# Performance work log

Measured on AMD Instinct MI355X. Metric: run time of the kernel, lower is better.

## Reference

```python
import jax, jax.numpy as jnp
import numpy as np

B, N, C, H, P = 16, 4096, 256, 4, 64  # batch, tokens, hidden, heads, proj_size
HD = C // H  # head dim = 64
EPS = 1e-12  # torch F.normalize eps


def _l2norm(t):
    # normalize along last axis, torch-style: t / max(||t||, eps)
    n = jnp.sqrt(jnp.sum(t * t, axis=-1, keepdims=True))
    return t / jnp.maximum(n, EPS)


def setup_inputs() -> dict:
    key = jax.random.key(0)
    ks = jax.random.split(key, 12)
    s = 0.02
    return {
        "x": jax.random.normal(ks[0], (B, N, C), jnp.float32),
        "ref": jax.random.normal(ks[1], (B, N, C), jnp.float32),
        "Wq": jax.random.normal(ks[2], (C, C), jnp.float32) * s,
        "bq": jnp.zeros((C,), jnp.float32),
        "Wkvv": jax.random.normal(ks[3], (3 * C, C), jnp.float32) * s,
        "bkvv": jnp.zeros((3 * C,), jnp.float32),
        "WE": jax.random.normal(ks[4], (P, N), jnp.float32) * s,  # E and F share weights
        "bE": jnp.zeros((P,), jnp.float32),
        "Wo1": jax.random.normal(ks[5], (C // 2, C), jnp.float32) * s,
        "bo1": jnp.zeros((C // 2,), jnp.float32),
        "Wo2": jax.random.normal(ks[6], (C // 2, C), jnp.float32) * s,
        "bo2": jnp.zeros((C // 2,), jnp.float32),
        "temp": jnp.ones((H, 1, 1), jnp.float32),
        "temp2": jnp.ones((H, 1, 1), jnp.float32),
    }


def reference(x, ref, Wq, bq, Wkvv, bkvv, WE, bE, Wo1, bo1, Wo2, bo2, temp, temp2):
    b, n, c = x.shape
    hd = c // H
    # q projection -> [B,H,hd,N] (already transposed so channel dim first)
    q = (x @ Wq.T + bq).reshape(b, n, H, hd).transpose(0, 2, 3, 1)
    kvv = (ref @ Wkvv.T + bkvv).reshape(b, n, 3, H, hd).transpose(2, 0, 3, 4, 1)
    k, v_ca, v_sa = kvv[0], kvv[1], kvv[2]
    # L2 normalize over token axis (last)
    qn = _l2norm(q)
    kn = _l2norm(k)
    # ---- channel attention (XCA-style): [B,H,hd,hd]
    attn_ca = jax.nn.softmax(jnp.einsum('bhcn,bhdn->bhcd', qn, kn) * temp, axis=-1)
    x_ca = jnp.einsum('bhcd,bhdn->bhcn', attn_ca, v_ca)  # [B,H,hd,N]
    x_ca = x_ca.transpose(0, 3, 1, 2).reshape(b, n, c)   # [B,N,C]
    # ---- spatial attention with Linformer-style projection (E == F shared)
    k_proj = kn @ WE.T + bE      # [B,H,hd,P]
    v_proj = v_sa @ WE.T + bE    # [B,H,hd,P]
    attn_sa = jax.nn.softmax(jnp.einsum('bhcn,bhcp->bhnp', qn, k_proj) * temp2, axis=-1)
    x_sa = jnp.einsum('bhnp,bhcp->bhnc', attn_sa, v_proj)  # [B,H,N,hd]
    # faithful to original permute(0,3,1,2).reshape(B,N,C)
    x_sa = x_sa.transpose(0, 3, 1, 2).reshape(b, n, c)
    # output projections + concat (SA first, then CA)
    out_ca = x_ca @ Wo1.T + bo1
    out_sa = x_sa @ Wo2.T + bo2
    return jnp.concatenate((out_sa, out_ca), axis=-1)
```

## Files before the change

kernel.cpp:

```cpp
#include <hip/hip_runtime.h>
#include <hip/hip_bf16.h>

#define DI __device__ __forceinline__

constexpr int B_ = 16, N_ = 4096, C_ = 256, H_ = 4;
constexpr size_t QSZ = (size_t)4096 * 4096;
constexpr int LDW = 72;
constexpr int LDC = 136;

typedef __attribute__((ext_vector_type(8))) short bh8;
typedef __attribute__((ext_vector_type(4))) float fx4;
typedef __attribute__((address_space(1))) unsigned int gu32;
typedef __attribute__((address_space(3))) unsigned int lu32;

DI float bfu2f(unsigned short u) { return __uint_as_float(((unsigned)u) << 16); }
DI void bfu2x2(unsigned u, float& lo, float& hi) {
  lo = __uint_as_float(u << 16);
  hi = __uint_as_float(u & 0xffff0000u);
}
DI unsigned short f2bfu(float f) {
  unsigned u = __float_as_uint(f);
  unsigned r = 0x7fffu + ((u >> 16) & 1u);
  return (unsigned short)((u + r) >> 16);
}
DI void gl_lds16(const unsigned short* g, unsigned short* l) {
  __builtin_amdgcn_global_load_lds((gu32*)g, (lu32*)l, 16, 0, 0);
}

__global__ __launch_bounds__(256) void cast_xref(
    const float* __restrict__ x, const float* __restrict__ ref,
    unsigned short* __restrict__ xb, unsigned short* __restrict__ refb)
{
  const int bid = blockIdx.x;
  const float* src = (bid < 8192) ? x : ref;
  unsigned short* dst = (bid < 8192) ? xb : refb;
  const size_t base = ((size_t)(bid & 8191) * 256 + threadIdx.x) * 8;
  const float4 a = *reinterpret_cast<const float4*>(&src[base]);
  const float4 b = *reinterpret_cast<const float4*>(&src[base + 4]);
  union { uint4 v; unsigned short u[8]; } pk;
  pk.u[0] = f2bfu(a.x); pk.u[1] = f2bfu(a.y); pk.u[2] = f2bfu(a.z); pk.u[3] = f2bfu(a.w);
  pk.u[4] = f2bfu(b.x); pk.u[5] = f2bfu(b.y); pk.u[6] = f2bfu(b.z); pk.u[7] = f2bfu(b.w);
  *reinterpret_cast<uint4*>(&dst[base]) = pk.v;
}

__global__ __launch_bounds__(256) void cast_w(
    const float* __restrict__ Wq, const float* __restrict__ Wkvv,
    const float* __restrict__ Wo2, const float* __restrict__ Wo1,
    const float* __restrict__ WE, unsigned short* __restrict__ Wb,
    unsigned short* __restrict__ wEb)
{
  const int b = blockIdx.x;
  const float* src; unsigned short* dst; int lb;
  if (b < 32)       { src = Wq;   dst = Wb;          lb = b; }
  else if (b < 128) { src = Wkvv; dst = Wb + 65536;  lb = b - 32; }
  else if (b < 144) { src = Wo2;  dst = Wb + 262144; lb = b - 128; }
  else if (b < 160) { src = Wo1;  dst = Wb + 294912; lb = b - 144; }
  else              { src = WE;   dst = wEb;         lb = b - 160; }
  const size_t base = ((size_t)lb * 256 + threadIdx.x) * 8;
  const float4 a = *reinterpret_cast<const float4*>(&src[base]);
  const float4 bb = *reinterpret_cast<const float4*>(&src[base + 4]);
  union { uint4 v; unsigned short u[8]; } pk;
  pk.u[0] = f2bfu(a.x);  pk.u[1] = f2bfu(a.y);  pk.u[2] = f2bfu(a.z);  pk.u[3] = f2bfu(a.w);
  pk.u[4] = f2bfu(bb.x); pk.u[5] = f2bfu(bb.y); pk.u[6] = f2bfu(bb.z); pk.u[7] = f2bfu(bb.w);
  *reinterpret_cast<uint4*>(&dst[base]) = pk.v;
}

__global__ __launch_bounds__(256) void proj_fused(
    const unsigned short* __restrict__ xb, const unsigned short* __restrict__ refb,
    const unsigned short* __restrict__ Wball,
    const float* __restrict__ bq, const float* __restrict__ bkvv,
    unsigned short* __restrict__ qT, unsigned short* __restrict__ kvv2T,
    unsigned short* __restrict__ qtok, unsigned short* __restrict__ vtok)
{
  __shared__ unsigned short smem[32768];
  __shared__ float biasS[128];
  const int tid = threadIdx.x;
  const int lane = tid & 63, wid = tid >> 6;
  const int l15 = lane & 15, l4 = lane >> 4;
  const int wr = wid >> 1, wc = wid & 1;
  const int yt = blockIdx.y;
  const bool isq = (yt < 2);
  const unsigned short* Ab = isq ? xb : refb;
  const unsigned short* Wsrc = isq ? Wball : (Wball + 65536);
  const float* bias = isq ? bq : bkvv;
  unsigned short* outT = isq ? qT : kvv2T;
  const int j0 = (isq ? yt : (yt - 2)) * 128;
  const int pl = j0 >> 8;
  const bool writeT = isq || (pl != 1);
  const int plT = (!isq && pl == 2) ? 1 : 0;
  unsigned short* tok = isq ? qtok : ((pl == 1) ? vtok : nullptr);
  const int n0 = blockIdx.x * 128;
  const int b = blockIdx.z;
  const size_t tok0 = (size_t)b * 4096 + n0;
  const int lrow = lane >> 3, lcb = lane & 7;
  if (tid < 128) biasS[tid] = bias[j0 + tid];

  fx4 acc[4][4];
#pragma unroll
  for (int m = 0; m < 4; ++m)
#pragma unroll
    for (int n = 0; n < 4; ++n) acc[m][n] = (fx4){0.f, 0.f, 0.f, 0.f};

  auto STAGE = [&](int buf, int k0) {
    unsigned short* Wd = smem + buf * 16384;
    unsigned short* Xd = Wd + 8192;
#pragma unroll
    for (int i = 0; i < 4; ++i) {
      const int ci = i * 4 + wid;
      const int row = ci * 8 + lrow;
      const int scb = lcb ^ (row & 7);
      gl_lds16(&Wsrc[(size_t)(j0 + row) * 256 + k0 + scb * 8], &Wd[ci * 512]);
      gl_lds16(&Ab[(tok0 + row) * 256 + k0 + scb * 8], &Xd[ci * 512]);
    }
  };
  auto COMPUTE = [&](int buf) {
    const unsigned short* Ws = smem + buf * 16384;
    const unsigned short* Xs = Ws + 8192;
#pragma unroll
    for (int kk = 0; kk < 2; ++kk) {
      const int cbi = kk * 4 + l4;
      bh8 af[4], bfr[4];
#pragma unroll
      for (int m = 0; m < 4; ++m) {
        const int r = wr * 64 + m * 16 + l15;
        af[m] = *reinterpret_cast<const bh8*>(&Ws[r * 64 + ((cbi ^ (r & 7)) << 3)]);
      }
#pragma unroll
      for (int n = 0; n < 4; ++n) {
        const int r = wc * 64 + n * 16 + l15;
        bfr[n] = *reinterpret_cast<const bh8*>(&Xs[r * 64 + ((cbi ^ (r & 7)) << 3)]);
      }
#pragma unroll
      for (int m = 0; m < 4; ++m)
#pragma unroll
        for (int n = 0; n < 4; ++n)
          acc[m][n] = __builtin_amdgcn_mfma_f32_16x16x32_bf16(af[m], bfr[n], acc[m][n], 0, 0, 0);
    }
  };

  STAGE(0, 0);
  __syncthreads();
  for (int t = 0; t < 4; ++t) {
    if (t < 3) STAGE((t + 1) & 1, (t + 1) * 64);
    COMPUTE(t & 1);
    __syncthreads();
  }

  unsigned short* Co = smem;
#pragma unroll
  for (int m = 0; m < 4; ++m) {
    const int jl = wr * 64 + m * 16 + (l4 << 2);
#pragma unroll
    for (int n = 0; n < 4; ++n) {
      const int col = wc * 64 + n * 16 + l15;
#pragma unroll
      for (int r = 0; r < 4; ++r)
        Co[(jl + r) * LDC + col] = f2bfu(acc[m][n][r] + biasS[jl + r]);
    }
  }
  __syncthreads();
  if (writeT) {
#pragma unroll
    for (int c = 0; c < 8; ++c) {
      const int r = c * 16 + (tid >> 4);
      const int colseg = (tid & 15) * 8;
      const uint4 v = *reinterpret_cast<const uint4*>(&Co[r * LDC + colseg]);
      const int jj = j0 + r;
      const int rowT = (plT * B_ + b) * 256 + (jj & 255);
      *reinterpret_cast<uint4*>(&outT[(size_t)rowT * N_ + n0 + colseg]) = v;
    }
  }
  if (tok) {
#pragma unroll
    for (int i = 0; i < 8; ++i) {
      const int half = i >> 2;
      const int cb = half * 64 + (tid & 7) * 8;
      const int nloc = (i & 3) * 32 + (tid >> 3);
      union { uint4 v; unsigned short u[8]; } pk;
#pragma unroll
      for (int t = 0; t < 8; ++t) pk.u[t] = Co[(cb + t) * LDC + nloc];
      const int jj = j0 + cb;
      const int hh = (jj >> 6) & 3, cc = jj & 63;
      *reinterpret_cast<uint4*>(
          &tok[(((size_t)b * 4 + hh) * 4096 + n0 + nloc) * 64 + cc]) = pk.v;
    }
  }
}

__global__ __launch_bounds__(256) void gemm_outm2(
    const unsigned short* __restrict__ Asa, const unsigned short* __restrict__ Aca,
    const unsigned short* __restrict__ Wob,
    const float* __restrict__ bo2, const float* __restrict__ bo1,
    float* __restrict__ out)
{
  __shared__ unsigned short smem[32768];
  __shared__ float biasS[128];
  const unsigned short* A = (blockIdx.z == 0) ? Asa : Aca;
  const unsigned short* Wsrc = Wob + (size_t)blockIdx.z * 32768;
  const float* bias = (blockIdx.z == 0) ? bo2 : bo1;
  const int joff = blockIdx.z * 128;
  const int tid = threadIdx.x;
  const int lane = tid & 63, wid = tid >> 6;
  const int l15 = lane & 15, l4 = lane >> 4;
  const int wr = wid >> 1, wc = wid & 1;
  const size_t m0 = (size_t)blockIdx.x * 128;
  const int lrow = lane >> 3, lcb = lane & 7;
  if (tid < 128) biasS[tid] = bias[tid];

  fx4 acc[4][4];
#pragma unroll
  for (int m = 0; m < 4; ++m)
#pragma unroll
    for (int n = 0; n < 4; ++n) acc[m][n] = (fx4){0.f, 0.f, 0.f, 0.f};

  auto STAGE = [&](int buf, int k0) {
    unsigned short* Wd = smem + buf * 16384;
    unsigned short* Xd = Wd + 8192;
#pragma unroll
    for (int i = 0; i < 4; ++i) {
      const int ci = i * 4 + wid;
      const int row = ci * 8 + lrow;
      const int scb = lcb ^ (row & 7);
      gl_lds16(&Wsrc[(size_t)row * 256 + k0 + scb * 8], &Wd[ci * 512]);
      gl_lds16(&A[(m0 + row) * 256 + k0 + scb * 8], &Xd[ci * 512]);
    }
  };
  auto COMPUTE = [&](int buf) {
    const unsigned short* Ws = smem + buf * 16384;
    const unsigned short* Xs = Ws + 8192;
#pragma unroll
    for (int kk = 0; kk < 2; ++kk) {
      const int cbi = kk * 4 + l4;
      bh8 af[4], bfr[4];
#pragma unroll
      for (int m = 0; m < 4; ++m) {
        const int r = wr * 64 + m * 16 + l15;
        af[m] = *reinterpret_cast<const bh8*>(&Xs[r * 64 + ((cbi ^ (r & 7)) << 3)]);
      }
#pragma unroll
      for (int n = 0; n < 4; ++n) {
        const int r = wc * 64 + n * 16 + l15;
        bfr[n] = *reinterpret_cast<const bh8*>(&Ws[r * 64 + ((cbi ^ (r & 7)) << 3)]);
      }
#pragma unroll
      for (int m = 0; m < 4; ++m)
#pragma unroll
        for (int n = 0; n < 4; ++n)
          acc[m][n] = __builtin_amdgcn_mfma_f32_16x16x32_bf16(af[m], bfr[n], acc[m][n], 0, 0, 0);
    }
  };

  STAGE(0, 0);
  __syncthreads();
  for (int t = 0; t < 4; ++t) {
    if (t < 3) STAGE((t + 1) & 1, (t + 1) * 64);
    COMPUTE(t & 1);
    __syncthreads();
  }

#pragma unroll
  for (int mi = 0; mi < 4; ++mi) {
    const int mrow = wr * 64 + mi * 16 + (l4 << 2);
#pragma unroll
    for (int ni = 0; ni < 4; ++ni) {
      const int j = wc * 64 + ni * 16 + l15;
      const float bv = biasS[j];
#pragma unroll
      for (int r = 0; r < 4; ++r)
        out[(m0 + mrow + r) * 256 + joff + j] = acc[mi][ni][r] + bv;
    }
  }
}

__global__ __launch_bounds__(256) void stats_mfma(
    const unsigned short* __restrict__ qT, const unsigned short* __restrict__ kT,
    const unsigned short* __restrict__ vT, const unsigned short* __restrict__ wEb,
    float* __restrict__ part, float* __restrict__ partN)
{
  __shared__ unsigned short smem[4 * 64 * LDW];
  unsigned short* sq = smem;
  unsigned short* sk = smem + 64 * LDW;
  unsigned short* sv = smem + 2 * 64 * LDW;
  unsigned short* sw = smem + 3 * 64 * LDW;
  const int tid = threadIdx.x;
  const int lane = tid & 63, wid = tid >> 6;
  const int bh = blockIdx.x, chunk = blockIdx.y;
  const size_t rowbase = (size_t)bh * 64 * N_;

  fx4 acc[4][4];
#pragma unroll
  for (int m = 0; m < 4; ++m)
#pragma unroll
    for (int n = 0; n < 4; ++n) acc[m][n] = (fx4){0.f, 0.f, 0.f, 0.f};
  float q2 = 0.f, k2 = 0.f;

  const unsigned short* Aop = (wid == 1) ? sw : (wid == 2) ? sv : sq;
  const unsigned short* Bop = (wid == 1) ? sk : (wid == 2) ? sw : sk;

  for (int tile = 0; tile < 8; ++tile) {
    const int n0 = chunk * 512 + tile * 64;
#pragma unroll
    for (int c = 0; c < 2; ++c) {
      const int idx = c * 256 + tid;
      const int r = idx >> 3;
      const int off = (idx & 7) * 8;
      *reinterpret_cast<uint4*>(&sq[r * LDW + off]) =
          *reinterpret_cast<const uint4*>(&qT[rowbase + (size_t)r * N_ + n0 + off]);
      *reinterpret_cast<uint4*>(&sk[r * LDW + off]) =
          *reinterpret_cast<const uint4*>(&kT[rowbase + (size_t)r * N_ + n0 + off]);
      *reinterpret_cast<uint4*>(&sv[r * LDW + off]) =
          *reinterpret_cast<const uint4*>(&vT[rowbase + (size_t)r * N_ + n0 + off]);
      *reinterpret_cast<uint4*>(&sw[r * LDW + off]) =
          *reinterpret_cast<const uint4*>(&wEb[(size_t)r * N_ + n0 + off]);
    }
    __syncthreads();
    if (wid < 3) {
#pragma unroll
      for (int kk = 0; kk < 2; ++kk) {
        const int kb = kk * 32 + (lane >> 4) * 8;
        bh8 af[4], bfr[4];
#pragma unroll
        for (int m = 0; m < 4; ++m)
          af[m] = *reinterpret_cast<const bh8*>(&Aop[(m * 16 + (lane & 15)) * LDW + kb]);
#pragma unroll
        for (int n = 0; n < 4; ++n)
          bfr[n] = *reinterpret_cast<const bh8*>(&Bop[(n * 16 + (lane & 15)) * LDW + kb]);
#pragma unroll
        for (int m = 0; m < 4; ++m)
#pragma unroll
          for (int n = 0; n < 4; ++n)
            acc[m][n] = __builtin_amdgcn_mfma_f32_16x16x32_bf16(af[m], bfr[n], acc[m][n], 0, 0, 0);
      }
    } else {
      const unsigned short* qrow = &sq[lane * LDW];
      const unsigned short* krow = &sk[lane * LDW];
#pragma unroll
      for (int t = 0; t < 8; ++t) {
        const uint4 uq = *reinterpret_cast<const uint4*>(&qrow[t * 8]);
        const uint4 uk = *reinterpret_cast<const uint4*>(&krow[t * 8]);
        float a, b;
        bfu2x2(uq.x, a, b); q2 += a * a + b * b;
        bfu2x2(uq.y, a, b); q2 += a * a + b * b;
        bfu2x2(uq.z, a, b); q2 += a * a + b * b;
        bfu2x2(uq.w, a, b); q2 += a * a + b * b;
        bfu2x2(uk.x, a, b); k2 += a * a + b * b;
        bfu2x2(uk.y, a, b); k2 += a * a + b * b;
        bfu2x2(uk.z, a, b); k2 += a * a + b * b;
        bfu2x2(uk.w, a, b); k2 += a * a + b * b;
      }
    }
    __syncthreads();
  }

  if (wid < 3) {
    float* base = &part[(((size_t)chunk * 64 + bh) * 3 + wid) * 4096];
#pragma unroll
    for (int m = 0; m < 4; ++m) {
      const int row0 = m * 16 + ((lane >> 4) << 2);
#pragma unroll
      for (int n = 0; n < 4; ++n) {
        const int col = n * 16 + (lane & 15);
#pragma unroll
        for (int r = 0; r < 4; ++r)
          base[(row0 + r) * 64 + col] = acc[m][n][r];
      }
    }
  } else {
    float* nb = &partN[((size_t)chunk * 64 + bh) * 128];
    nb[lane] = q2;
    nb[64 + lane] = k2;
  }
}

__global__ __launch_bounds__(256) void postproc_kernel(
    const float* __restrict__ part, const float* __restrict__ partN,
    const float* __restrict__ bE,
    const float* __restrict__ temp, const float* __restrict__ temp2,
    unsigned short* __restrict__ attn_b,
    unsigned short* __restrict__ kp2t, unsigned short* __restrict__ vpb)
{
  __shared__ float sums[12288];
  __shared__ float rqS[64], rkS[64];
  const int bh = blockIdx.x;
  const int tid = threadIdx.x;
  for (int idx = tid; idx < 12288; idx += 256) {
    float s = 0.f;
    for (int ch = 0; ch < 8; ++ch)
      s += part[((size_t)ch * 64 + bh) * 12288 + idx];
    sums[idx] = s;
  }
  if (tid < 128) {
    float s = 0.f;
    for (int ch = 0; ch < 8; ++ch)
      s += partN[((size_t)ch * 64 + bh) * 128 + tid];
    const float r = 1.f / fmaxf(sqrtf(s), 1e-12f);
    if (tid < 64) rqS[tid] = r; else rkS[tid - 64] = r;
  }
  __syncthreads();
  const float t2 = temp2[bh & 3];
  for (int idx = tid; idx < 4096; idx += 256) {
    const int p = idx >> 6, c = idx & 63;
    kp2t[(size_t)bh * 4096 + idx] =
        f2bfu((sums[4096 + idx] * rkS[c] + bE[p]) * rqS[c] * t2);
    vpb[(size_t)bh * 4096 + idx] = f2bfu(sums[8192 + idx] + bE[idx & 63]);
  }
  const float tv = temp[bh & 3];
  const int lane = tid & 63, wv = tid >> 6;
  for (int ri = 0; ri < 16; ++ri) {
    const int c = wv * 16 + ri;
    const float val = sums[c * 64 + lane] * rqS[c] * rkS[lane] * tv;
    float m = val;
#pragma unroll
    for (int off = 32; off > 0; off >>= 1) m = fmaxf(m, __shfl_xor(m, off));
    const float e = __expf(val - m);
    float ssum = e;
#pragma unroll
    for (int off = 32; off > 0; off >>= 1) ssum += __shfl_xor(ssum, off);
    attn_b[(size_t)bh * 4096 + c * 64 + lane] = f2bfu(e / ssum);
  }
}

__global__ __launch_bounds__(256) void sa_mfma(
    const unsigned short* __restrict__ qtok, const unsigned short* __restrict__ kp2t,
    const unsigned short* __restrict__ vpb, unsigned short* __restrict__ x_sa)
{
  __shared__ unsigned short skp[64 * LDW];
  __shared__ unsigned short svp[64 * LDW];
  __shared__ unsigned short pt[4][64 * LDW];
  const int tid = threadIdx.x;
  const int lane = tid & 63, wid = tid >> 6;
  const int l15 = lane & 15, l4 = lane >> 4;
  const int bh = blockIdx.x, b = bh >> 2, h = bh & 3;
  const int n0 = blockIdx.y * 256 + wid * 64;
  unsigned short* myp = &pt[wid][0];

#pragma unroll
  for (int i = 0; i < 2; ++i) {
    const int idx = i * 256 + tid;
    const int r = idx >> 3, off = (idx & 7) * 8;
    *reinterpret_cast<uint4*>(&skp[r * LDW + off]) =
        *reinterpret_cast<const uint4*>(&kp2t[(size_t)bh * 4096 + r * 64 + off]);
    *reinterpret_cast<uint4*>(&svp[r * LDW + off]) =
        *reinterpret_cast<const uint4*>(&vpb[(size_t)bh * 4096 + r * 64 + off]);
  }
  __syncthreads();

  fx4 acc[4][4];
#pragma unroll
  for (int m = 0; m < 4; ++m)
#pragma unroll
    for (int j = 0; j < 4; ++j) acc[m][j] = (fx4){0.f, 0.f, 0.f, 0.f};
  const size_t qbase = ((size_t)bh * 4096 + n0) * 64;
#pragma unroll
  for (int kk = 0; kk < 2; ++kk) {
    const int kb = kk * 32 + l4 * 8;
    bh8 af[4], bf[4];
#pragma unroll
    for (int m = 0; m < 4; ++m)
      af[m] = *reinterpret_cast<const bh8*>(&qtok[qbase + (size_t)(m * 16 + l15) * 64 + kb]);
#pragma unroll
    for (int j = 0; j < 4; ++j)
      bf[j] = *reinterpret_cast<const bh8*>(&skp[(j * 16 + l15) * LDW + kb]);
#pragma unroll
    for (int m = 0; m < 4; ++m)
#pragma unroll
      for (int j = 0; j < 4; ++j)
        acc[m][j] = __builtin_amdgcn_mfma_f32_16x16x32_bf16(af[m], bf[j], acc[m][j], 0, 0, 0);
  }

  fx4 inv[4];
#pragma unroll
  for (int m = 0; m < 4; ++m) {
    fx4 vm = acc[m][0];
#pragma unroll
    for (int j = 1; j < 4; ++j)
#pragma unroll
      for (int r = 0; r < 4; ++r) vm[r] = fmaxf(vm[r], acc[m][j][r]);
#pragma unroll
    for (int msk = 1; msk < 16; msk <<= 1)
#pragma unroll
      for (int r = 0; r < 4; ++r) vm[r] = fmaxf(vm[r], __shfl_xor(vm[r], msk));
    fx4 s = (fx4){0.f, 0.f, 0.f, 0.f};
#pragma unroll
    for (int j = 0; j < 4; ++j)
#pragma unroll
      for (int r = 0; r < 4; ++r) {
        acc[m][j][r] = __expf(acc[m][j][r] - vm[r]);
        s[r] += acc[m][j][r];
      }
#pragma unroll
    for (int msk = 1; msk < 16; msk <<= 1)
#pragma unroll
      for (int r = 0; r < 4; ++r) s[r] += __shfl_xor(s[r], msk);
#pragma unroll
    for (int r = 0; r < 4; ++r) inv[m][r] = 1.f / s[r];
#pragma unroll
    for (int j = 0; j < 4; ++j)
#pragma unroll
      for (int r = 0; r < 4; ++r)
        myp[(m * 16 + l4 * 4 + r) * LDW + j * 16 + l15] = f2bfu(acc[m][j][r]);
  }

  fx4 acc2[4][4];
#pragma unroll
  for (int m = 0; m < 4; ++m)
#pragma unroll
    for (int j = 0; j < 4; ++j) acc2[m][j] = (fx4){0.f, 0.f, 0.f, 0.f};
#pragma unroll
  for (int kk = 0; kk < 2; ++kk) {
    const int kb = kk * 32 + l4 * 8;
    bh8 af[4], bf[4];
#pragma unroll
    for (int m = 0; m < 4; ++m)
      af[m] = *reinterpret_cast<const bh8*>(&myp[(m * 16 + l15) * LDW + kb]);
#pragma unroll
    for (int j = 0; j < 4; ++j)
      bf[j] = *reinterpret_cast<const bh8*>(&svp[(j * 16 + l15) * LDW + kb]);
#pragma unroll
    for (int m = 0; m < 4; ++m)
#pragma unroll
      for (int j = 0; j < 4; ++j)
        acc2[m][j] = __builtin_amdgcn_mfma_f32_16x16x32_bf16(af[m], bf[j], acc2[m][j], 0, 0, 0);
  }

#pragma unroll
  for (int m = 0; m < 4; ++m)
#pragma unroll
    for (int j = 0; j < 4; ++j)
#pragma unroll
      for (int r = 0; r < 4; ++r)
        myp[(m * 16 + l4 * 4 + r) * 65 + j * 16 + l15] = f2bfu(acc2[m][j][r] * inv[m][r]);
#pragma unroll
  for (int dstep = 0; dstep < 8; ++dstep) {
    const int d = dstep * 8 + (lane >> 3);
    const int nseg = (lane & 7) * 8;
    union { uint4 v; unsigned short u[8]; } pk;
#pragma unroll
    for (int t = 0; t < 8; ++t) pk.u[t] = myp[(nseg + t) * 65 + d];
    *reinterpret_cast<uint4*>(
        &x_sa[((size_t)(b * 64 + d) * 4 + h) * (size_t)N_ + n0 + nseg]) = pk.v;
  }
}

__global__ __launch_bounds__(256) void xca_mfma(
    const unsigned short* __restrict__ attn_b, const unsigned short* __restrict__ vtok,
    unsigned short* __restrict__ x_ca)
{
  __shared__ unsigned short co[4][64 * LDW];
  const int tid = threadIdx.x;
  const int lane = tid & 63, wid = tid >> 6;
  const int l15 = lane & 15, l4 = lane >> 4;
  const int bh = blockIdx.x, b = bh >> 2, h = bh & 3;
  const int n0 = blockIdx.y * 256 + wid * 64;
  unsigned short* myco = &co[wid][0];

  fx4 acc[4][4];
#pragma unroll
  for (int m = 0; m < 4; ++m)
#pragma unroll
    for (int j = 0; j < 4; ++j) acc[m][j] = (fx4){0.f, 0.f, 0.f, 0.f};
  const size_t abase = (size_t)bh * 4096;
  const size_t vbase = ((size_t)bh * 4096 + n0) * 64;
#pragma unroll
  for (int kk = 0; kk < 2; ++kk) {
    const int kb = kk * 32 + l4 * 8;
    bh8 af[4], bf[4];
#pragma unroll
    for (int m = 0; m < 4; ++m)
      af[m] = *reinterpret_cast<const bh8*>(&attn_b[abase + (size_t)(m * 16 + l15) * 64 + kb]);
#pragma unroll
    for (int j = 0; j < 4; ++j)
      bf[j] = *reinterpret_cast<const bh8*>(&vtok[vbase + (size_t)(j * 16 + l15) * 64 + kb]);
#pragma unroll
    for (int m = 0; m < 4; ++m)
#pragma unroll
      for (int j = 0; j < 4; ++j)
        acc[m][j] = __builtin_amdgcn_mfma_f32_16x16x32_bf16(af[m], bf[j], acc[m][j], 0, 0, 0);
  }

#pragma unroll
  for (int m = 0; m < 4; ++m)
#pragma unroll
    for (int j = 0; j < 4; ++j)
#pragma unroll
      for (int r = 0; r < 4; ++r)
        myco[(j * 16 + l15) * LDW + m * 16 + l4 * 4 + r] = f2bfu(acc[m][j][r]);
#pragma unroll
  for (int p = 0; p < 8; ++p) {
    const int nloc = p * 8 + (lane >> 3);
    const int cseg = (lane & 7) * 8;
    const uint4 v = *reinterpret_cast<const uint4*>(&myco[nloc * LDW + cseg]);
    *reinterpret_cast<uint4*>(
        &x_ca[((size_t)b * N_ + n0 + nloc) * 256 + h * 64 + cseg]) = v;
  }
}

extern "C" void kernel_launch(void* const* d_in, const int* in_sizes, int n_in,
                              void* d_out, int out_size, void* d_ws, size_t ws_size,
                              hipStream_t stream)
{
  const float* x     = (const float*)d_in[0];
  const float* ref   = (const float*)d_in[1];
  const float* Wq    = (const float*)d_in[2];
  const float* bq    = (const float*)d_in[3];
  const float* Wkvv  = (const float*)d_in[4];
  const float* bkvv  = (const float*)d_in[5];
  const float* WE    = (const float*)d_in[6];
  const float* bE    = (const float*)d_in[7];
  const float* Wo1   = (const float*)d_in[8];
  const float* bo1   = (const float*)d_in[9];
  const float* Wo2   = (const float*)d_in[10];
  const float* bo2   = (const float*)d_in[11];
  const float* temp  = (const float*)d_in[12];
  const float* temp2 = (const float*)d_in[13];
  float* out = (float*)d_out;

  char* ws = (char*)d_ws;
  unsigned short* qT      = (unsigned short*)(ws);
  unsigned short* kvv2T   = (unsigned short*)(ws + 33554432);
  unsigned short* qtok    = (unsigned short*)(ws + 100663296);
  unsigned short* refb    = (unsigned short*)(ws + 134217728);
  unsigned short* x_sa    = (unsigned short*)(ws + 134217728);
  unsigned short* vca_tok = (unsigned short*)(ws + 167772160);
  unsigned short* xb      = (unsigned short*)(ws + 201326592);
  float*          part    = (float*)(ws + 201326592);
  unsigned short* x_ca    = (unsigned short*)(ws + 201326592);
  float*          partN   = (float*)(ws + 226492416);
  unsigned short* Wb      = (unsigned short*)(ws + 234881024);
  unsigned short* wEb     = (unsigned short*)(ws + 235536384);
  unsigned short* attn_b  = (unsigned short*)(ws + 236093440);
  unsigned short* kp2t    = (unsigned short*)(ws + 236617728);
  unsigned short* vpb     = (unsigned short*)(ws + 237142016);

  const dim3 blk(256);
  cast_xref<<<dim3(16384), blk, 0, stream>>>(x, ref, xb, refb);
  cast_w<<<dim3(288), blk, 0, stream>>>(Wq, Wkvv, Wo2, Wo1, WE, Wb, wEb);
  proj_fused<<<dim3(32, 8, 16), blk, 0, stream>>>(xb, refb, Wb, bq, bkvv,
                                                  qT, kvv2T, qtok, vca_tok);
  stats_mfma<<<dim3(64, 8), blk, 0, stream>>>(qT, kvv2T, kvv2T + QSZ, wEb, part, partN);
  postproc_kernel<<<dim3(64), blk, 0, stream>>>(part, partN, bE, temp, temp2,
                                                attn_b, kp2t, vpb);
  sa_mfma<<<dim3(64, 16), blk, 0, stream>>>(qtok, kp2t, vpb, x_sa);
  xca_mfma<<<dim3(64, 16), blk, 0, stream>>>(attn_b, vca_tok, x_ca);
  gemm_outm2<<<dim3(512, 1, 2), blk, 0, stream>>>(x_sa, x_ca, Wb + 262144, bo2, bo1, out);
}
```

Before: 213.4 us.

## Halve LDS footprint in projection GEMMs with K=32 tiles and chunked epilogue

Both projection GEMM kernels now stage K-slices of 32 instead of 64, which halves shared memory per block from 64KB to 32KB, with a new XOR swizzle for the narrower rows. The proj_fused epilogue writes the output tile through LDS in two 64-row halves, using a swizzled layout to reduce bank conflicts on the transposed reads. The aim is higher occupancy (more resident blocks per CU) to hide latency. The cost is twice as many K-loop iterations and barriers, plus extra barriers in the epilogue.

After: 259.5 us. 21.6% more time.

```diff
diff --git a/kernel.cpp b/kernel.cpp
--- a/kernel.cpp
+++ b/kernel.cpp
@@ -26,6 +26,8 @@
 DI void gl_lds16(const unsigned short* g, unsigned short* l) {
   __builtin_amdgcn_global_load_lds((gu32*)g, (lu32*)l, 16, 0, 0);
 }
+DI int key4(int row) { return (row ^ (row >> 2)) & 3; }
+DI int key8(int row) { return ((row >> 3) ^ row) & 7; }
 
 __global__ __launch_bounds__(256) void cast_xref(
     const float* __restrict__ x, const float* __restrict__ ref,
@@ -72,7 +74,7 @@
     unsigned short* __restrict__ qT, unsigned short* __restrict__ kvv2T,
     unsigned short* __restrict__ qtok, unsigned short* __restrict__ vtok)
 {
-  __shared__ unsigned short smem[32768];
+  __shared__ unsigned short smem[16384];
   __shared__ float biasS[128];
   const int tid = threadIdx.x;
   const int lane = tid & 63, wid = tid >> 6;
@@ -92,7 +94,6 @@
   const int n0 = blockIdx.x * 128;
   const int b = blockIdx.z;
   const size_t tok0 = (size_t)b * 4096 + n0;
-  const int lrow = lane >> 3, lcb = lane & 7;
   if (tid < 128) biasS[tid] = bias[j0 + tid];
 
   fx4 acc[4][4];
@@ -102,87 +103,94 @@
     for (int n = 0; n < 4; ++n) acc[m][n] = (fx4){0.f, 0.f, 0.f, 0.f};
 
   auto STAGE = [&](int buf, int k0) {
-    unsigned short* Wd = smem + buf * 16384;
-    unsigned short* Xd = Wd + 8192;
-#pragma unroll
-    for (int i = 0; i < 4; ++i) {
-      const int ci = i * 4 + wid;
-      const int row = ci * 8 + lrow;
-      const int scb = lcb ^ (row & 7);
-      gl_lds16(&Wsrc[(size_t)(j0 + row) * 256 + k0 + scb * 8], &Wd[ci * 512]);
-      gl_lds16(&Ab[(tok0 + row) * 256 + k0 + scb * 8], &Xd[ci * 512]);
+    unsigned short* Wd = smem + buf * 8192;
+    unsigned short* Xd = Wd + 4096;
+#pragma unroll
+    for (int i = 0; i < 2; ++i) {
+      const int sb = (i * 4 + wid) * 64;
+      const int row = (sb >> 2) + (lane >> 2);
+      const int soct = (lane & 3) ^ key4(row);
+      gl_lds16(&Wsrc[(size_t)(j0 + row) * 256 + k0 + soct * 8], &Wd[sb * 8]);
+      gl_lds16(&Ab[(tok0 + row) * 256 + k0 + soct * 8], &Xd[sb * 8]);
     }
   };
   auto COMPUTE = [&](int buf) {
-    const unsigned short* Ws = smem + buf * 16384;
-    const unsigned short* Xs = Ws + 8192;
-#pragma unroll
-    for (int kk = 0; kk < 2; ++kk) {
-      const int cbi = kk * 4 + l4;
-      bh8 af[4], bfr[4];
-#pragma unroll
-      for (int m = 0; m < 4; ++m) {
-        const int r = wr * 64 + m * 16 + l15;
-        af[m] = *reinterpret_cast<const bh8*>(&Ws[r * 64 + ((cbi ^ (r & 7)) << 3)]);
-      }
-#pragma unroll
-      for (int n = 0; n < 4; ++n) {
-        const int r = wc * 64 + n * 16 + l15;
-        bfr[n] = *reinterpret_cast<const bh8*>(&Xs[r * 64 + ((cbi ^ (r & 7)) << 3)]);
-      }
-#pragma unroll
-      for (int m = 0; m < 4; ++m)
-#pragma unroll
-        for (int n = 0; n < 4; ++n)
-          acc[m][n] = __builtin_amdgcn_mfma_f32_16x16x32_bf16(af[m], bfr[n], acc[m][n], 0, 0, 0);
-    }
+    const unsigned short* Ws = smem + buf * 8192;
+    const unsigned short* Xs = Ws + 4096;
+    bh8 af[4], bfr[4];
+#pragma unroll
+    for (int m = 0; m < 4; ++m) {
+      const int r = wr * 64 + m * 16 + l15;
+      af[m] = *reinterpret_cast<const bh8*>(&Ws[r * 32 + ((l4 ^ key4(r)) << 3)]);
+    }
+#pragma unroll
+    for (int n = 0; n < 4; ++n) {
+      const int r = wc * 64 + n * 16 + l15;
+      bfr[n] = *reinterpret_cast<const bh8*>(&Xs[r * 32 + ((l4 ^ key4(r)) << 3)]);
+    }
+#pragma unroll
+    for (int m = 0; m < 4; ++m)
+#pragma unroll
+      for (int n = 0; n < 4; ++n)
+        acc[m][n] = __builtin_amdgcn_mfma_f32_16x16x32_bf16(af[m], bfr[n], acc[m][n], 0, 0, 0);
   };
 
   STAGE(0, 0);
   __syncthreads();
-  for (int t = 0; t < 4; ++t) {
-    if (t < 3) STAGE((t + 1) & 1, (t + 1) * 64);
+  for (int t = 0; t < 8; ++t) {
+    if (t < 7) STAGE((t + 1) & 1, (t + 1) * 32);
     COMPUTE(t & 1);
     __syncthreads();
   }
 
   unsigned short* Co = smem;
-#pragma unroll
-  for (int m = 0; m < 4; ++m) {
-    const int jl = wr * 64 + m * 16 + (l4 << 2);
-#pragma unroll
-    for (int n = 0; n < 4; ++n) {
-      const int col = wc * 64 + n * 16 + l15;
-#pragma unroll
-      for (int r = 0; r < 4; ++r)
-        Co[(jl + r) * LDC + col] = f2bfu(acc[m][n][r] + biasS[jl + r]);
-    }
-  }
-  __syncthreads();
-  if (writeT) {
-#pragma unroll
-    for (int c = 0; c < 8; ++c) {
-      const int r = c * 16 + (tid >> 4);
-      const int colseg = (tid & 15) * 8;
-      const uint4 v = *reinterpret_cast<const uint4*>(&Co[r * LDC + colseg]);
-      const int jj = j0 + r;
-      const int rowT = (plT * B_ + b) * 256 + (jj & 255);
-      *reinterpret_cast<uint4*>(&outT[(size_t)rowT * N_ + n0 + colseg]) = v;
-    }
-  }
-  if (tok) {
-#pragma unroll
-    for (int i = 0; i < 8; ++i) {
-      const int half = i >> 2;
-      const int cb = half * 64 + (tid & 7) * 8;
-      const int nloc = (i & 3) * 32 + (tid >> 3);
-      union { uint4 v; unsigned short u[8]; } pk;
-#pragma unroll
-      for (int t = 0; t < 8; ++t) pk.u[t] = Co[(cb + t) * LDC + nloc];
-      const int jj = j0 + cb;
-      const int hh = (jj >> 6) & 3, cc = jj & 63;
-      *reinterpret_cast<uint4*>(
-          &tok[(((size_t)b * 4 + hh) * 4096 + n0 + nloc) * 64 + cc]) = pk.v;
+  for (int jh = 0; jh < 2; ++jh) {
+    __syncthreads();
+    if (wr == jh) {
+#pragma unroll
+      for (int m = 0; m < 4; ++m) {
+        const int rl = m * 16 + (l4 << 2);
+#pragma unroll
+        for (int n = 0; n < 4; ++n) {
+          const int col = wc * 64 + n * 16 + l15;
+#pragma unroll
+          for (int r = 0; r < 4; ++r) {
+            const int row = rl + r;
+            const int p = (col >> 3) ^ key8(row);
+            Co[row * LDC + p * 8 + (col & 7)] = f2bfu(acc[m][n][r] + biasS[jh * 64 + row]);
+          }
+        }
+      }
+    }
+    __syncthreads();
+    if (writeT) {
+#pragma unroll
+      for (int c = 0; c < 4; ++c) {
+        const int row = c * 16 + (tid >> 4);
+        const int o = tid & 15;
+        const uint4 v = *reinterpret_cast<const uint4*>(&Co[row * LDC + ((o ^ key8(row)) << 3)]);
+        const int jj = j0 + jh * 64 + row;
+        const int rowT = (plT * B_ + b) * 256 + (jj & 255);
+        *reinterpret_cast<uint4*>(&outT[(size_t)rowT * N_ + n0 + o * 8]) = v;
+      }
+    }
+    if (tok) {
+      const int jj = j0 + jh * 64;
+      const int hh = (jj >> 6) & 3;
+#pragma unroll
+      for (int i = 0; i < 4; ++i) {
+        const int nloc = i * 32 + (tid >> 3);
+        const int o = tid & 7;
+        union { uint4 v; unsigned short u[8]; } pk;
+#pragma unroll
+        for (int tt = 0; tt < 8; ++tt) {
+          const int row = o * 8 + tt;
+          const int p = (nloc >> 3) ^ key8(row);
+          pk.u[tt] = Co[row * LDC + p * 8 + (nloc & 7)];
+        }
+        *reinterpret_cast<uint4*>(
+            &tok[(((size_t)b * 4 + hh) * 4096 + n0 + nloc) * 64 + o * 8]) = pk.v;
+      }
     }
   }
 }
@@ -193,7 +201,7 @@
     const float* __restrict__ bo2, const float* __restrict__ bo1,
     float* __restrict__ out)
 {
-  __shared__ unsigned short smem[32768];
+  __shared__ unsigned short smem[16384];
   __shared__ float biasS[128];
   const unsigned short* A = (blockIdx.z == 0) ? Asa : Aca;
   const unsigned short* Wsrc = Wob + (size_t)blockIdx.z * 32768;
@@ -204,7 +212,6 @@
   const int l15 = lane & 15, l4 = lane >> 4;
   const int wr = wid >> 1, wc = wid & 1;
   const size_t m0 = (size_t)blockIdx.x * 128;
-  const int lrow = lane >> 3, lcb = lane & 7;
   if (tid < 128) biasS[tid] = bias[tid];
 
   fx4 acc[4][4];
@@ -214,46 +221,42 @@
     for (int n = 0; n < 4; ++n) acc[m][n] = (fx4){0.f, 0.f, 0.f, 0.f};
 
   auto STAGE = [&](int buf, int k0) {
-    unsigned short* Wd = smem + buf * 16384;
-    unsigned short* Xd = Wd + 8192;
-#pragma unroll
-    for (int i = 0; i < 4; ++i) {
-      const int ci = i * 4 + wid;
-      const int row = ci * 8 + lrow;
-      const int scb = lcb ^ (row & 7);
-      gl_lds16(&Wsrc[(size_t)row * 256 + k0 + scb * 8], &Wd[ci * 512]);
-      gl_lds16(&A[(m0 + row) * 256 + k0 + scb * 8], &Xd[ci * 512]);
+    unsigned short* Wd = smem + buf * 8192;
+    unsigned short* Xd = Wd + 4096;
+#pragma unroll
+    for (int i = 0; i < 2; ++i) {
+      const int sb = (i * 4 + wid) * 64;
+      const int row = (sb >> 2) + (lane >> 2);
+      const int soct = (lane & 3) ^ key4(row);
+      gl_lds16(&Wsrc[(size_t)row * 256 + k0 + soct * 8], &Wd[sb * 8]);
+      gl_lds16(&A[(m0 + row) * 256 + k0 + soct * 8], &Xd[sb * 8]);
     }
   };
   auto COMPUTE = [&](int buf) {
-    const unsigned short* Ws = smem + buf * 16384;
-    const unsigned short* Xs = Ws + 8192;
-#pragma unroll
-    for (int kk = 0; kk < 2; ++kk) {
-      const int cbi = kk * 4 + l4;
-      bh8 af[4], bfr[4];
-#pragma unroll
-      for (int m = 0; m < 4; ++m) {
-        const int r = wr * 64 + m * 16 + l15;
-        af[m] = *reinterpret_cast<const bh8*>(&Xs[r * 64 + ((cbi ^ (r & 7)) << 3)]);
-      }
-#pragma unroll
-      for (int n = 0; n < 4; ++n) {
-        const int r = wc * 64 + n * 16 + l15;
-        bfr[n] = *reinterpret_cast<const bh8*>(&Ws[r * 64 + ((cbi ^ (r & 7)) << 3)]);
-      }
-#pragma unroll
-      for (int m = 0; m < 4; ++m)
-#pragma unroll
-        for (int n = 0; n < 4; ++n)
-          acc[m][n] = __builtin_amdgcn_mfma_f32_16x16x32_bf16(af[m], bfr[n], acc[m][n], 0, 0, 0);
-    }
+    const unsigned short* Ws = smem + buf * 8192;
+    const unsigned short* Xs = Ws + 4096;
+    bh8 af[4], bfr[4];
+#pragma unroll
+    for (int m = 0; m < 4; ++m) {
+      const int r = wr * 64 + m * 16 + l15;
+      af[m] = *reinterpret_cast<const bh8*>(&Xs[r * 32 + ((l4 ^ key4(r)) << 3)]);
+    }
+#pragma unroll
+    for (int n = 0; n < 4; ++n) {
+      const int r = wc * 64 + n * 16 + l15;
+      bfr[n] = *reinterpret_cast<const bh8*>(&Ws[r * 32 + ((l4 ^ key4(r)) << 3)]);
+    }
+#pragma unroll
+    for (int m = 0; m < 4; ++m)
+#pragma unroll
+      for (int n = 0; n < 4; ++n)
+        acc[m][n] = __builtin_amdgcn_mfma_f32_16x16x32_bf16(af[m], bfr[n], acc[m][n], 0, 0, 0);
   };
 
   STAGE(0, 0);
   __syncthreads();
-  for (int t = 0; t < 4; ++t) {
-    if (t < 3) STAGE((t + 1) & 1, (t + 1) * 64);
+  for (int t = 0; t < 8; ++t) {
+    if (t < 7) STAGE((t + 1) & 1, (t + 1) * 32);
     COMPUTE(t & 1);
     __syncthreads();
   }
```
